# Kernel optimization log

Measured on AMD Instinct MI355X. Metric: run time of the kernel, lower is better.

Reference implementation:

```python
import jax, jax.numpy as jnp
import numpy as np
from jax import lax

F = 8  # db4 filter length
_DEC_LO = np.array([-0.010597401784997278, 0.032883011666982945,
                    0.030841381835986965, -0.18703481171888114,
                    -0.02798376941698385, 0.6308807679295904,
                    0.7148465705525415, 0.23037781330885523], dtype=np.float32)
_DEC_HI = np.array([(-1.0) ** (k + 1) * _DEC_LO[k] for k in range(F)], dtype=np.float32)
_REC_LO = _DEC_LO[::-1].copy()
_REC_HI = _DEC_HI[::-1].copy()
# lax.conv is cross-correlation; flip filters to get np.convolve semantics.
DEC_KERN = jnp.asarray(np.stack([_DEC_LO[::-1], _DEC_HI[::-1]])[:, None, :])   # [2,1,F]
REC_KERN = jnp.asarray(np.stack([_REC_LO[::-1], _REC_HI[::-1]])[None, :, :])   # [1,2,F]
REC_LO_KERN = jnp.asarray(_REC_LO[::-1][None, None, :])                        # [1,1,F]


def dwt1(x):
    """Single-level db4 DWT, pywt/ptwt 'reflect' mode. x:[N,L] -> (lp,hp) each [N, floor((L+F-1)/2)]."""
    xp = jnp.pad(x, ((0, 0), (F - 1, F - 1)), mode='reflect')[:, 1:]
    y = lax.conv_general_dilated(xp[:, None, :], DEC_KERN,
                                 window_strides=(2,), padding='VALID')
    return y[:, 0], y[:, 1]


def idwt(ca, cd, out_len):
    """Single-level inverse db4 DWT (pywt waverec step): out_len = 2*C - F + 2."""
    u = jnp.stack([ca, cd], axis=1)  # [N,2,C]
    y = lax.conv_general_dilated(u, REC_KERN, window_strides=(1,),
                                 padding=[(F - 1, F - 1)], lhs_dilation=(2,))
    return y[:, 0, F - 2:F - 2 + out_len]


def idwt_lo(ca, out_len):
    """Inverse DWT with zero detail coefficients (baseline upsampling)."""
    y = lax.conv_general_dilated(ca[:, None, :], REC_LO_KERN, window_strides=(1,),
                                 padding=[(F - 1, F - 1)], lhs_dilation=(2,))
    return y[:, 0, F - 2:F - 2 + out_len]


def calculate_baseline(s):
    """s:[N,L]. Iterative lowpass pyramid with per-row SSD local-minimum stopping rule.
    The torch version shrinks the active row set; here we keep the full batch and track a
    per-row stop depth, which provably yields identical results (depths are set at most once,
    and the torch data-dependent 'all stopped' break only skips unused computation)."""
    N = s.shape[0]
    sigs = [s]
    ssds = []
    depth = jnp.full((N,), -1, dtype=jnp.int32)
    t = 0
    while True:  # static unroll: bounded by (lp length < 8) or (iter > 7)
        lp, hp = dwt1(sigs[t])
        ssds.append(jnp.sum(hp * hp, axis=-1))
        if t >= 2:
            newly = (ssds[t - 2] > ssds[t - 1]) & (ssds[t - 1] < ssds[t]) & (depth < 0)
            depth = jnp.where(newly, t, depth)
            if lp.shape[-1] < 8 or t > 7:
                break
        sigs.append(lp)
        t += 1
    depth = jnp.where(depth < 0, t, depth)  # rows never stopped keep the deepest level
    bl = sigs[-1]
    for k in range(len(sigs) - 2, -1, -1):
        rec = idwt_lo(bl, sigs[k].shape[-1])  # waverec([lp, zeros]) + odd-length trim
        bl = jnp.where((depth >= k + 1)[:, None], rec, sigs[k])
    return bl


def f_remove_baseline(x):
    s = x.reshape(-1, x.shape[-1])
    bl = calculate_baseline(s).reshape(x.shape)
    return x - lax.stop_gradient(bl)  # torch detaches the baseline


def f_remove_hf_noise(x):
    s = x.reshape(-1, x.shape[-1])
    ca, details = s, []
    for _ in range(4):  # level = 4
        ca, cd = dwt1(ca)
        details.append(cd)  # [cD1, cD2, cD3, cD4]
    flat = jnp.sort(jnp.abs(details[-1]).ravel())
    sigma = flat[(flat.shape[0] - 1) // 2] / jnp.float32(0.6745)  # torch.median = lower middle
    details = [jnp.where(d < sigma, jnp.float32(0), d) for d in details]  # signed threshold, as in source
    for cd in reversed(details):
        if ca.shape[-1] == cd.shape[-1] + 1:
            ca = ca[:, :-1]
        ca = idwt(ca, cd, 2 * cd.shape[-1] - F + 2)
    return ca.reshape(x.shape)


def f_normalize(x):
    mean = jnp.mean(x, axis=-1, keepdims=True)
    std = jnp.std(x, axis=-1, keepdims=True, ddof=1)  # torch.std_mean is unbiased
    return jnp.nan_to_num((x - mean) / std)


def setup_inputs() -> dict:
    key = jax.random.key(0)
    x = jax.random.normal(key, (512, 12, 5000), dtype=jnp.float32)
    return {"x": x}


def reference(x):
    x = f_remove_baseline(x)
    x = f_remove_hf_noise(x)
    x = f_normalize(x)  # result_only=True: std/mean aux outputs are discarded
    return x
```

## Files before the change

kernel.cpp:

```cpp
#include <hip/hip_runtime.h>
#include <math.h>

#define NROWS 6144
#define LSIG  5000
#define NT    256

#define DL0 (-0.010597401784997278f)
#define DL1 ( 0.032883011666982945f)
#define DL2 ( 0.030841381835986965f)
#define DL3 (-0.18703481171888114f)
#define DL4 (-0.02798376941698385f)
#define DL5 ( 0.6308807679295904f)
#define DL6 ( 0.7148465705525415f)
#define DL7 ( 0.23037781330885523f)
#define DH0 ( 0.010597401784997278f)
#define DH1 ( 0.032883011666982945f)
#define DH2 (-0.030841381835986965f)
#define DH3 (-0.18703481171888114f)
#define DH4 ( 0.02798376941698385f)
#define DH5 ( 0.6308807679295904f)
#define DH6 (-0.7148465705525415f)
#define DH7 ( 0.23037781330885523f)

__device__ __forceinline__ void dwt_pair_edge(const float* __restrict__ src, int L, int k,
                                              float& a, float& b) {
    const float LO[8] = {DL0,DL1,DL2,DL3,DL4,DL5,DL6,DL7};
    const float HI[8] = {DH0,DH1,DH2,DH3,DH4,DH5,DH6,DH7};
    a = 0.f; b = 0.f;
    int base = 2*k - 6;
#pragma unroll
    for (int t = 0; t < 8; ++t) {
        int j = base + t;
        int i = (j < 0) ? -j : j;
        if (i >= L) i = 2*L - 2 - i;
        float v = src[i];
        a += v * LO[7-t];
        b += v * HI[7-t];
    }
}

__device__ __forceinline__ void dwt_pair_int(const float* __restrict__ src, int k,
                                             float& a, float& b) {
    int base = 2*k - 6;
    const float2* s2 = (const float2*)(src + base);
    float2 p0 = s2[0], p1 = s2[1], p2 = s2[2], p3 = s2[3];
    float v0 = p0.x, v1 = p0.y, v2 = p1.x, v3 = p1.y;
    float v4 = p2.x, v5 = p2.y, v6 = p3.x, v7 = p3.y;
    a = v0*DL7 + v1*DL6 + v2*DL5 + v3*DL4 + v4*DL3 + v5*DL2 + v6*DL1 + v7*DL0;
    b = v0*DH7 + v1*DH6 + v2*DH5 + v3*DH4 + v4*DH3 + v5*DH2 + v6*DH1 + v7*DH0;
}

__device__ __forceinline__ void idwt_lo_pair(const float* __restrict__ ca, int m,
                                             float& ev, float& od) {
    float c0 = ca[m], c1 = ca[m+1], c2 = ca[m+2], c3 = ca[m+3];
    ev = c0*DL1 + c1*DL3 + c2*DL5 + c3*DL7;
    od = c0*DL0 + c1*DL2 + c2*DL4 + c3*DL6;
}

__global__ __launch_bounds__(NT, 4) void kernelA(const float* __restrict__ x,
                                                 float* __restrict__ g_d1, float* __restrict__ g_d2,
                                                 float* __restrict__ g_d3, float* __restrict__ g_d4,
                                                 float* __restrict__ g_ca4,
                                                 unsigned* __restrict__ bins,
                                                 unsigned* __restrict__ state) {
    __shared__ float sig0[5000];
    __shared__ float pyr[5040];
    __shared__ float redm[9][4];
    __shared__ int depth_s;

    const int row = blockIdx.x;
    const int tid = threadIdx.x;

    if (row == 0) {
        for (int i = tid; i < 2048; i += NT) bins[i] = 0u;
        if (tid == 0) { state[0] = 0u; state[1] = 979967u; }
    }

    {
        const float4* xr4 = (const float4*)(x + (size_t)row * LSIG);
        float4* s4 = (float4*)sig0;
        for (int i = tid; i < 1250; i += NT) s4[i] = xr4[i];
    }
    __syncthreads();

    const int lensA[10] = {5000, 2503, 1255, 631, 319, 163, 85, 46, 26, 16};
    const int offs[8]   = {0, 2504, 3760, 4392, 4712, 4876, 4962, 5008};

    float sp[9];
    const float* src = sig0;
#pragma unroll
    for (int t = 0; t < 9; ++t) {
        const int L   = lensA[t];
        const int Lo  = lensA[t + 1];
        const int kHi = (L - 2) >> 1;
        float* lp = pyr + ((t < 8) ? offs[t] : 0);
        float part = 0.f;
        for (int k = tid; k < Lo; k += NT) {
            float a, b;
            if (k >= 3 && k <= kHi) dwt_pair_int(src, k, a, b);
            else                    dwt_pair_edge(src, L, k, a, b);
            if (t < 8) lp[k] = a;
            part += b * b;
        }
        sp[t] = part;
        __syncthreads();
        src = lp;
    }

#pragma unroll
    for (int t = 0; t < 9; ++t) {
        float p = sp[t];
#pragma unroll
        for (int o = 32; o; o >>= 1) p += __shfl_down(p, o, 64);
        if ((tid & 63) == 0) redm[t][tid >> 6] = p;
    }
    __syncthreads();
    if (tid == 0) {
        float ssds[9];
#pragma unroll
        for (int t = 0; t < 9; ++t) ssds[t] = redm[t][0] + redm[t][1] + redm[t][2] + redm[t][3];
        int dd = -1;
        for (int t = 2; t <= 8; ++t)
            if (dd < 0 && ssds[t - 2] > ssds[t - 1] && ssds[t - 1] < ssds[t]) dd = t;
        depth_s = (dd < 0) ? 8 : dd;
    }
    __syncthreads();
    const int d = depth_s;

    const float* cur = pyr + offs[d - 1];
    for (int k = d - 1; k >= 1; --k) {
        const int ol = lensA[k];
        float* dst = (k & 1) ? pyr : (pyr + 2504);
        const int np = (ol + 1) >> 1;
        for (int m = tid; m < np; m += NT) {
            float ev, od;
            idwt_lo_pair(cur, m, ev, od);
            dst[2*m] = ev;
            if (2*m + 1 < ol) dst[2*m + 1] = od;
        }
        __syncthreads();
        cur = dst;
    }
    for (int q = tid; q < 1250; q += NT) {
        const int m = 2 * q;
        const float2* c2p = (const float2*)(cur + m);
        float2 ca01 = c2p[0], ca23 = c2p[1];
        float c0 = ca01.x, c1 = ca01.y, c2 = ca23.x, c3 = ca23.y, c4 = cur[m+4];
        float ev0 = c0*DL1 + c1*DL3 + c2*DL5 + c3*DL7;
        float od0 = c0*DL0 + c1*DL2 + c2*DL4 + c3*DL6;
        float ev1 = c1*DL1 + c2*DL3 + c3*DL5 + c4*DL7;
        float od1 = c1*DL0 + c2*DL2 + c3*DL4 + c4*DL6;
        sig0[2*m]     -= ev0;
        sig0[2*m + 1] -= od0;
        sig0[2*m + 2] -= ev1;
        sig0[2*m + 3] -= od1;
    }
    __syncthreads();

    const int l2[5] = {5000, 2503, 1255, 631, 319};
    src = sig0;
#pragma unroll
    for (int lev = 0; lev < 4; ++lev) {
        const int L   = l2[lev];
        const int Lo  = l2[lev + 1];
        const int kHi = (L - 2) >> 1;
        float* lp = pyr + ((lev & 1) ? 2504 : 0);
        float* hg;
        if      (lev == 0) hg = g_d1 + (size_t)row * 2503;
        else if (lev == 1) hg = g_d2 + (size_t)row * 1255;
        else if (lev == 2) hg = g_d3 + (size_t)row * 631;
        else               hg = g_d4 + (size_t)row * 319;
        for (int k = tid; k < Lo; k += NT) {
            float a, b;
            if (k >= 3 && k <= kHi) dwt_pair_int(src, k, a, b);
            else                    dwt_pair_edge(src, L, k, a, b);
            lp[k] = a;
            hg[k] = b;
        }
        __syncthreads();
        src = lp;
    }
    float* cg = g_ca4 + (size_t)row * 319;
    for (int i = tid; i < 319; i += NT) cg[i] = pyr[2504 + i];
}

__global__ void khist(const float* __restrict__ data, int n, unsigned* __restrict__ bins,
                      const unsigned* __restrict__ state, int shift, unsigned binmask,
                      unsigned prefmask) {
    __shared__ unsigned h[2048];
    const int nb = (int)binmask + 1;
    for (int i = threadIdx.x; i < nb; i += blockDim.x) h[i] = 0u;
    __syncthreads();
    const unsigned pref = state[0] & prefmask;
    const int stride = gridDim.x * blockDim.x;
    for (int i = blockIdx.x * blockDim.x + threadIdx.x; i < n; i += stride) {
        unsigned key = __float_as_uint(fabsf(data[i]));
        if ((key & prefmask) == pref) atomicAdd(&h[(key >> shift) & binmask], 1u);
    }
    __syncthreads();
    for (int i = threadIdx.x; i < nb; i += blockDim.x)
        if (h[i]) atomicAdd(&bins[i], h[i]);
}

__global__ void kselect(unsigned* bins, unsigned* state,
                        float* sigma_out, int shift, int nbins, int final_pass) {
    __shared__ unsigned sb[2048];
    __shared__ unsigned cs[256];
    const int tid = threadIdx.x;
    const int CH  = nbins >> 8;
    unsigned sum = 0;
    for (int j = 0; j < CH; ++j) {
        unsigned v = bins[tid * CH + j];
        sb[tid * CH + j] = v;
        sum += v;
    }
    cs[tid] = sum;
    __syncthreads();
    if (tid == 0) {
        const unsigned krem = state[1];
        unsigned cum = 0;
        int ch = 0;
        for (; ch < 256; ++ch) {
            unsigned c = cs[ch];
            if (cum + c > krem) break;
            cum += c;
        }
        int b;
        if (ch == 256) {
            b = nbins - 1;
            cum -= sb[nbins - 1];
        } else {
            b = ch * CH;
            for (; b < nbins - 1; ++b) {
                unsigned c = sb[b];
                if (cum + c > krem) break;
                cum += c;
            }
        }
        unsigned prefix = state[0] | ((unsigned)b << shift);
        state[0] = prefix;
        state[1] = krem - cum;
        if (final_pass) *sigma_out = __uint_as_float(prefix) / 0.6745f;
    }
    __syncthreads();
    for (int i = tid; i < nbins; i += 256) bins[i] = 0u;
}

__global__ __launch_bounds__(NT, 4) void kernelC(const float* __restrict__ g_d1,
                                                 const float* __restrict__ g_d2,
                                                 const float* __restrict__ g_d3,
                                                 const float* __restrict__ g_d4,
                                                 const float* __restrict__ g_ca4,
                                                 const float* __restrict__ sigma_p,
                                                 float* __restrict__ out) {
    __shared__ float A[5000];
    __shared__ float B[2504];
    __shared__ float Dd[2504];
    __shared__ double redd[4][2];
    __shared__ float sg;

    const int row = blockIdx.x;
    const int tid = threadIdx.x;
    if (tid == 0) sg = *sigma_p;
    for (int i = tid; i < 319; i += NT) A[i] = g_ca4[(size_t)row * 319 + i];
    __syncthreads();
    const float sigma = sg;

    const int Cs[4] = {319, 631, 1255, 2503};
    const int Os[4] = {632, 1256, 2504, 5000};

#pragma unroll
    for (int s = 0; s < 4; ++s) {
        const int C = Cs[s];
        const int O = Os[s];
        const float* dg;
        if      (s == 0) dg = g_d4 + (size_t)row * 319;
        else if (s == 1) dg = g_d3 + (size_t)row * 631;
        else if (s == 2) dg = g_d2 + (size_t)row * 1255;
        else             dg = g_d1 + (size_t)row * 2503;
        const float* spb = (s & 1) ? B : A;
        float* dp        = (s & 1) ? A : B;
        for (int i = tid; i < C; i += NT) {
            float v = dg[i];
            Dd[i] = (v < sigma) ? 0.f : v;
        }
        __syncthreads();
        const int nq = O >> 2;
        for (int q = tid; q < nq; q += NT) {
            const int m = 2 * q;
            const float2* cp = (const float2*)(spb + m);
            const float2* ep = (const float2*)(Dd + m);
            float2 cA = cp[0], cB = cp[1];
            float2 eA = ep[0], eB = ep[1];
            float c0 = cA.x, c1 = cA.y, c2 = cB.x, c3 = cB.y, c4 = spb[m+4];
            float e0 = eA.x, e1 = eA.y, e2 = eB.x, e3 = eB.y, e4 = Dd[m+4];
            float s0 = c0 + e0, s1 = c1 + e1, s2 = c2 + e2, s3 = c3 + e3, s4 = c4 + e4;
            float u0 = c0 - e0, u1 = c1 - e1, u2 = c2 - e2, u3 = c3 - e3, u4 = c4 - e4;
            float ev0 = s0*DL1 + s1*DL3 + s2*DL5 + s3*DL7;
            float od0 = u0*DL0 + u1*DL2 + u2*DL4 + u3*DL6;
            float ev1 = s1*DL1 + s2*DL3 + s3*DL5 + s4*DL7;
            float od1 = u1*DL0 + u2*DL2 + u3*DL4 + u4*DL6;
            dp[2*m]     = ev0;
            dp[2*m + 1] = od0;
            dp[2*m + 2] = ev1;
            dp[2*m + 3] = od1;
        }
        __syncthreads();
    }

    double s1 = 0.0, s2 = 0.0;
    for (int i = tid; i < 5000; i += NT) {
        double v = (double)A[i];
        s1 += v;
        s2 += v * v;
    }
#pragma unroll
    for (int o = 32; o; o >>= 1) {
        s1 += __shfl_down(s1, o, 64);
        s2 += __shfl_down(s2, o, 64);
    }
    if ((tid & 63) == 0) { redd[tid >> 6][0] = s1; redd[tid >> 6][1] = s2; }
    __syncthreads();
    double sum  = redd[0][0] + redd[1][0] + redd[2][0] + redd[3][0];
    double sumq = redd[0][1] + redd[1][1] + redd[2][1] + redd[3][1];
    double mean = sum / 5000.0;
    double var  = (sumq - sum * mean) / 4999.0;

    float meanf = (float)mean;
    float inv = 1.0f / (float)sqrt(var);
    float* orow = out + (size_t)row * 5000;
    for (int i = tid; i < 5000; i += NT) {
        float r = (A[i] - meanf) * inv;
        if (isnan(r)) r = 0.f;
        else if (isinf(r)) r = copysignf(3.4028234663852886e38f, r);
        orow[i] = r;
    }
}

extern "C" void kernel_launch(void* const* d_in, const int* in_sizes, int n_in,
                              void* d_out, int out_size, void* d_ws, size_t ws_size,
                              hipStream_t stream) {
    const float* x = (const float*)d_in[0];
    float* out = (float*)d_out;

    const size_t n1 = (size_t)NROWS * 2503;
    const size_t n2 = (size_t)NROWS * 1255;
    const size_t n3 = (size_t)NROWS * 631;
    const size_t n4 = (size_t)NROWS * 319;

    float* w    = (float*)d_ws;
    float* d1   = w;
    float* d2   = d1 + n1;
    float* d3   = d2 + n2;
    float* d4   = d3 + n3;
    float* ca4  = d4 + n4;
    unsigned* bins  = (unsigned*)(ca4 + n4);
    unsigned* state = bins + 2048;
    float* sigp = (float*)(state + 2);
    const int n = (int)n4;

    hipLaunchKernelGGL(kernelA, dim3(NROWS), dim3(NT), 0, stream, x, d1, d2, d3, d4, ca4, bins, state);
    hipLaunchKernelGGL(khist, dim3(512), dim3(256), 0, stream, d4, n, bins, state, 21, 2047u, 0x00000000u);
    hipLaunchKernelGGL(kselect, dim3(1), dim3(256), 0, stream, bins, state, sigp, 21, 2048, 0);
    hipLaunchKernelGGL(khist, dim3(512), dim3(256), 0, stream, d4, n, bins, state, 10, 2047u, 0xFFE00000u);
    hipLaunchKernelGGL(kselect, dim3(1), dim3(256), 0, stream, bins, state, sigp, 10, 2048, 0);
    hipLaunchKernelGGL(khist, dim3(512), dim3(256), 0, stream, d4, n, bins, state, 0, 1023u, 0xFFFFFC00u);
    hipLaunchKernelGGL(kselect, dim3(1), dim3(256), 0, stream, bins, state, sigp, 0, 1024, 1);
    hipLaunchKernelGGL(kernelC, dim3(NROWS), dim3(NT), 0, stream, d1, d2, d3, d4, ca4, sigp, out);
}
```

Baseline: 413.5 us.

## Fuse histogram and select passes via last-block pattern; vectorize histogram loads

Merges each histogram pass with its selection step into one kernel: the last block to finish, detected through an atomic counter, does the bin scan. This removes three kernel launches. The histogram now reads float4 values and uses 256 blocks. The inverse-transform loops in kernelA and kernelC switch from two output pairs per thread to one pair per thread, giving more parallelism but less register reuse. The risk is relying on __threadfence and atomic reads for correct cross-block visibility.

```diff
diff --git a/kernel.cpp b/kernel.cpp
--- a/kernel.cpp
+++ b/kernel.cpp
@@ -73,7 +73,7 @@
 
     if (row == 0) {
         for (int i = tid; i < 2048; i += NT) bins[i] = 0u;
-        if (tid == 0) { state[0] = 0u; state[1] = 979967u; }
+        if (tid == 0) { state[0] = 0u; state[1] = 979967u; state[2] = 0u; }
     }
 
     {
@@ -141,19 +141,11 @@
         __syncthreads();
         cur = dst;
     }
-    for (int q = tid; q < 1250; q += NT) {
-        const int m = 2 * q;
-        const float2* c2p = (const float2*)(cur + m);
-        float2 ca01 = c2p[0], ca23 = c2p[1];
-        float c0 = ca01.x, c1 = ca01.y, c2 = ca23.x, c3 = ca23.y, c4 = cur[m+4];
-        float ev0 = c0*DL1 + c1*DL3 + c2*DL5 + c3*DL7;
-        float od0 = c0*DL0 + c1*DL2 + c2*DL4 + c3*DL6;
-        float ev1 = c1*DL1 + c2*DL3 + c3*DL5 + c4*DL7;
-        float od1 = c1*DL0 + c2*DL2 + c3*DL4 + c4*DL6;
-        sig0[2*m]     -= ev0;
-        sig0[2*m + 1] -= od0;
-        sig0[2*m + 2] -= ev1;
-        sig0[2*m + 3] -= od1;
+    for (int m = tid; m < 2500; m += NT) {
+        float ev, od;
+        idwt_lo_pair(cur, m, ev, od);
+        sig0[2*m]     -= ev;
+        sig0[2*m + 1] -= od;
     }
     __syncthreads();
 
@@ -184,34 +176,49 @@
     for (int i = tid; i < 319; i += NT) cg[i] = pyr[2504 + i];
 }
 
-__global__ void khist(const float* __restrict__ data, int n, unsigned* __restrict__ bins,
-                      const unsigned* __restrict__ state, int shift, unsigned binmask,
-                      unsigned prefmask) {
+__global__ void khsel(const float4* __restrict__ data4, int n4,
+                      unsigned* __restrict__ bins, unsigned* __restrict__ state,
+                      float* __restrict__ sigma_out, int shift, unsigned binmask,
+                      unsigned prefmask, int final_pass) {
     __shared__ unsigned h[2048];
-    const int nb = (int)binmask + 1;
-    for (int i = threadIdx.x; i < nb; i += blockDim.x) h[i] = 0u;
+    __shared__ unsigned cs[256];
+    __shared__ int lastFlag;
+    const int nb  = (int)binmask + 1;
+    const int tid = threadIdx.x;
+
+    for (int i = tid; i < nb; i += 256) h[i] = 0u;
     __syncthreads();
     const unsigned pref = state[0] & prefmask;
-    const int stride = gridDim.x * blockDim.x;
-    for (int i = blockIdx.x * blockDim.x + threadIdx.x; i < n; i += stride) {
-        unsigned key = __float_as_uint(fabsf(data[i]));
-        if ((key & prefmask) == pref) atomicAdd(&h[(key >> shift) & binmask], 1u);
-    }
-    __syncthreads();
-    for (int i = threadIdx.x; i < nb; i += blockDim.x)
+    const int stride = gridDim.x * 256;
+    for (int i = blockIdx.x * 256 + tid; i < n4; i += stride) {
+        float4 v = data4[i];
+        unsigned k0 = __float_as_uint(fabsf(v.x));
+        unsigned k1 = __float_as_uint(fabsf(v.y));
+        unsigned k2 = __float_as_uint(fabsf(v.z));
+        unsigned k3 = __float_as_uint(fabsf(v.w));
+        if ((k0 & prefmask) == pref) atomicAdd(&h[(k0 >> shift) & binmask], 1u);
+        if ((k1 & prefmask) == pref) atomicAdd(&h[(k1 >> shift) & binmask], 1u);
+        if ((k2 & prefmask) == pref) atomicAdd(&h[(k2 >> shift) & binmask], 1u);
+        if ((k3 & prefmask) == pref) atomicAdd(&h[(k3 >> shift) & binmask], 1u);
+    }
+    __syncthreads();
+    for (int i = tid; i < nb; i += 256)
         if (h[i]) atomicAdd(&bins[i], h[i]);
-}
-
-__global__ void kselect(unsigned* bins, unsigned* state,
-                        float* sigma_out, int shift, int nbins, int final_pass) {
-    __shared__ unsigned sb[2048];
-    __shared__ unsigned cs[256];
-    const int tid = threadIdx.x;
-    const int CH  = nbins >> 8;
+    __syncthreads();
+
+    if (tid == 0) {
+        __threadfence();
+        unsigned t = atomicAdd(&state[2], 1u);
+        lastFlag = (t == gridDim.x - 1) ? 1 : 0;
+    }
+    __syncthreads();
+    if (!lastFlag) return;
+
+    const int CH = nb >> 8;
     unsigned sum = 0;
     for (int j = 0; j < CH; ++j) {
-        unsigned v = bins[tid * CH + j];
-        sb[tid * CH + j] = v;
+        unsigned v = atomicAdd(&bins[tid * CH + j], 0u);
+        h[tid * CH + j] = v;
         sum += v;
     }
     cs[tid] = sum;
@@ -227,12 +234,12 @@
         }
         int b;
         if (ch == 256) {
-            b = nbins - 1;
-            cum -= sb[nbins - 1];
+            b = nb - 1;
+            cum -= h[nb - 1];
         } else {
             b = ch * CH;
-            for (; b < nbins - 1; ++b) {
-                unsigned c = sb[b];
+            for (; b < nb - 1; ++b) {
+                unsigned c = h[b];
                 if (cum + c > krem) break;
                 cum += c;
             }
@@ -240,10 +247,11 @@
         unsigned prefix = state[0] | ((unsigned)b << shift);
         state[0] = prefix;
         state[1] = krem - cum;
+        state[2] = 0u;
         if (final_pass) *sigma_out = __uint_as_float(prefix) / 0.6745f;
     }
     __syncthreads();
-    for (int i = tid; i < nbins; i += 256) bins[i] = 0u;
+    for (int i = tid; i < nb; i += 256) bins[i] = 0u;
 }
 
 __global__ __launch_bounds__(NT, 4) void kernelC(const float* __restrict__ g_d1,
@@ -285,25 +293,14 @@
             Dd[i] = (v < sigma) ? 0.f : v;
         }
         __syncthreads();
-        const int nq = O >> 2;
-        for (int q = tid; q < nq; q += NT) {
-            const int m = 2 * q;
-            const float2* cp = (const float2*)(spb + m);
-            const float2* ep = (const float2*)(Dd + m);
-            float2 cA = cp[0], cB = cp[1];
-            float2 eA = ep[0], eB = ep[1];
-            float c0 = cA.x, c1 = cA.y, c2 = cB.x, c3 = cB.y, c4 = spb[m+4];
-            float e0 = eA.x, e1 = eA.y, e2 = eB.x, e3 = eB.y, e4 = Dd[m+4];
-            float s0 = c0 + e0, s1 = c1 + e1, s2 = c2 + e2, s3 = c3 + e3, s4 = c4 + e4;
-            float u0 = c0 - e0, u1 = c1 - e1, u2 = c2 - e2, u3 = c3 - e3, u4 = c4 - e4;
-            float ev0 = s0*DL1 + s1*DL3 + s2*DL5 + s3*DL7;
-            float od0 = u0*DL0 + u1*DL2 + u2*DL4 + u3*DL6;
-            float ev1 = s1*DL1 + s2*DL3 + s3*DL5 + s4*DL7;
-            float od1 = u1*DL0 + u2*DL2 + u3*DL4 + u4*DL6;
-            dp[2*m]     = ev0;
-            dp[2*m + 1] = od0;
-            dp[2*m + 2] = ev1;
-            dp[2*m + 3] = od1;
+        const int np = O >> 1;
+        for (int m = tid; m < np; m += NT) {
+            float c0 = spb[m], c1 = spb[m+1], c2 = spb[m+2], c3 = spb[m+3];
+            float e0 = Dd[m],  e1 = Dd[m+1],  e2 = Dd[m+2],  e3 = Dd[m+3];
+            float s0 = c0 + e0, s1 = c1 + e1, s2 = c2 + e2, s3 = c3 + e3;
+            float u0 = c0 - e0, u1 = c1 - e1, u2 = c2 - e2, u3 = c3 - e3;
+            dp[2*m]     = s0*DL1 + s1*DL3 + s2*DL5 + s3*DL7;
+            dp[2*m + 1] = u0*DL0 + u1*DL2 + u2*DL4 + u3*DL6;
         }
         __syncthreads();
     }
@@ -356,15 +353,15 @@
     float* ca4  = d4 + n4;
     unsigned* bins  = (unsigned*)(ca4 + n4);
     unsigned* state = bins + 2048;
-    float* sigp = (float*)(state + 2);
-    const int n = (int)n4;
+    float* sigp = (float*)(state + 4);
+    const int nq4 = (int)(n4 / 4);
 
     hipLaunchKernelGGL(kernelA, dim3(NROWS), dim3(NT), 0, stream, x, d1, d2, d3, d4, ca4, bins, state);
-    hipLaunchKernelGGL(khist, dim3(512), dim3(256), 0, stream, d4, n, bins, state, 21, 2047u, 0x00000000u);
-    hipLaunchKernelGGL(kselect, dim3(1), dim3(256), 0, stream, bins, state, sigp, 21, 2048, 0);
-    hipLaunchKernelGGL(khist, dim3(512), dim3(256), 0, stream, d4, n, bins, state, 10, 2047u, 0xFFE00000u);
-    hipLaunchKernelGGL(kselect, dim3(1), dim3(256), 0, stream, bins, state, sigp, 10, 2048, 0);
-    hipLaunchKernelGGL(khist, dim3(512), dim3(256), 0, stream, d4, n, bins, state, 0, 1023u, 0xFFFFFC00u);
-    hipLaunchKernelGGL(kselect, dim3(1), dim3(256), 0, stream, bins, state, sigp, 0, 1024, 1);
+    hipLaunchKernelGGL(khsel, dim3(256), dim3(256), 0, stream, (const float4*)d4, nq4,
+                       bins, state, sigp, 21, 2047u, 0x00000000u, 0);
+    hipLaunchKernelGGL(khsel, dim3(256), dim3(256), 0, stream, (const float4*)d4, nq4,
+                       bins, state, sigp, 10, 2047u, 0xFFE00000u, 0);
+    hipLaunchKernelGGL(khsel, dim3(256), dim3(256), 0, stream, (const float4*)d4, nq4,
+                       bins, state, sigp, 0, 1023u, 0xFFFFFC00u, 1);
     hipLaunchKernelGGL(kernelC, dim3(NROWS), dim3(NT), 0, stream, d1, d2, d3, d4, ca4, sigp, out);
 }
```

Measured after the change: 408.0 us. Within noise of the previous version (-1.3%).
